# Performance work log

Hardware: AMD Instinct MI355X
Metric: run time of the kernel (lower is better)

## Reference

```python
import jax, jax.numpy as jnp
import numpy as np

N = 100000
E = 1600000
G = 2048          # number of graphs in the batch
HEADS = 4
HID = 16          # per-head channels
IN_CH = 128
D = HEADS * HID   # 64, concat output width per layer
NEG_SLOPE = 0.2


def _gat_layer(x, src, dst, W, a_src, a_dst, bias):
    # x: [N, Fin], W: [Fin, H*C], a_src/a_dst: [H, C], bias: [H*C]
    h = (x @ W).reshape(N, HEADS, HID)                      # [N, H, C]
    al_s = jnp.einsum('nhc,hc->nh', h, a_src)               # [N, H]
    al_d = jnp.einsum('nhc,hc->nh', h, a_dst)               # [N, H]
    e = jax.nn.leaky_relu(al_s[src] + al_d[dst], NEG_SLOPE) # [E+N, H]
    # segment softmax over incoming edges of each destination node
    m = jax.ops.segment_max(e, dst, num_segments=N)         # [N, H]
    e = jnp.exp(e - m[dst])
    s = jax.ops.segment_sum(e, dst, num_segments=N)
    alpha = e / (s[dst] + 1e-16)                            # [E+N, H]
    msg = h[src] * alpha[..., None]                         # [E+N, H, C]
    out = jax.ops.segment_sum(msg, dst, num_segments=N)     # [N, H, C]
    return out.reshape(N, D) + bias


def setup_inputs() -> dict:
    key = jax.random.key(0)
    ks = jax.random.split(key, 16)
    x = jax.random.normal(ks[0], (N, IN_CH), dtype=jnp.float32)
    edge_index = jax.random.randint(ks[1], (2, E), 0, N, dtype=jnp.int64)
    batch = jnp.sort(jax.random.randint(ks[2], (N,), 0, G, dtype=jnp.int64))
    inp = {'x': x, 'edge_index': edge_index, 'batch': batch}
    fins = [IN_CH, D, D]
    for i, fin in enumerate(fins):
        kk = jax.random.split(ks[3 + i], 4)
        sc = 1.0 / np.sqrt(fin)
        inp[f'W{i}'] = jax.random.normal(kk[0], (fin, D), dtype=jnp.float32) * sc
        inp[f'as{i}'] = jax.random.normal(kk[1], (HEADS, HID), dtype=jnp.float32) * 0.1
        inp[f'ad{i}'] = jax.random.normal(kk[2], (HEADS, HID), dtype=jnp.float32) * 0.1
        inp[f'b{i}'] = jnp.zeros((D,), dtype=jnp.float32)
    inp['head_w'] = jax.random.normal(ks[10], (1, D), dtype=jnp.float32) * (1.0 / np.sqrt(D))
    inp['head_b'] = jnp.zeros((1,), dtype=jnp.float32)
    return inp


def reference(x, edge_index, batch,
              W0, as0, ad0, b0,
              W1, as1, ad1, b1,
              W2, as2, ad2, b2,
              head_w, head_b):
    # PyG GATConv adds self-loops by default
    loops = jnp.arange(N, dtype=edge_index.dtype)
    src = jnp.concatenate([edge_index[0], loops])
    dst = jnp.concatenate([edge_index[1], loops])
    layers = [(W0, as0, ad0, b0), (W1, as1, ad1, b1), (W2, as2, ad2, b2)]
    h = x.astype(jnp.float32)
    for (W, a_s, a_d, b) in layers:
        h = _gat_layer(h, src, dst, W, a_s, a_d, b)
        h = jax.nn.relu(h)  # dropout p=0.0 -> identity
    pooled = jax.ops.segment_sum(h, batch, num_segments=G)  # [G, D]
    out = pooled @ head_w.T + head_b                         # [G, 1]
    return out.reshape(-1)                                   # out_dim == 1 -> flatten
```

## Files before the change

### kernel.cpp

```cpp
#include <hip/hip_runtime.h>
#include <hip/hip_bf16.h>
#include <cstdint>
#include <cstddef>

#define NN 100000
#define EE 1600000
#define GG 2048
#define EN (EE + NN)

constexpr int NB_SCAN = (NN + 255) / 256;

__device__ __forceinline__ float lrelu(float v) { return v > 0.f ? v : 0.2f * v; }

__global__ void k_count(const int* __restrict__ ei, int* __restrict__ deg,
                        int* __restrict__ rank) {
    int i = blockIdx.x * blockDim.x + threadIdx.x;
    if (i >= EN) return;
    int d = (i < EE) ? ei[EE + i] : (i - EE);
    rank[i] = atomicAdd(&deg[d], 1);
}

__global__ void k_scan1(const int* __restrict__ deg, int* __restrict__ offs,
                        int* __restrict__ bsums) {
    __shared__ int tmp[256];
    int tid = threadIdx.x;
    int i = blockIdx.x * 256 + tid;
    int v = (i < NN) ? deg[i] : 0;
    tmp[tid] = v; __syncthreads();
    for (int off = 1; off < 256; off <<= 1) {
        int t = (tid >= off) ? tmp[tid - off] : 0;
        __syncthreads();
        tmp[tid] += t;
        __syncthreads();
    }
    if (i < NN) offs[i] = tmp[tid] - v;
    if (tid == 255) bsums[blockIdx.x] = tmp[255];
}

__global__ void k_scan2(int* __restrict__ bsums) {
    __shared__ int tmp[512];
    int tid = threadIdx.x;
    int v = (tid < NB_SCAN) ? bsums[tid] : 0;
    tmp[tid] = v; __syncthreads();
    for (int off = 1; off < 512; off <<= 1) {
        int t = (tid >= off) ? tmp[tid - off] : 0;
        __syncthreads();
        tmp[tid] += t;
        __syncthreads();
    }
    if (tid < NB_SCAN) bsums[tid] = tmp[tid] - v;
}

__global__ void k_scan3(int* __restrict__ offs, const int* __restrict__ bsums) {
    int i = blockIdx.x * 256 + threadIdx.x;
    if (i < NN) offs[i] += bsums[blockIdx.x];
}

__global__ void k_scatter(const int* __restrict__ ei, const int* __restrict__ offs,
                          const int* __restrict__ rank, int* __restrict__ col) {
    int i = blockIdx.x * blockDim.x + threadIdx.x;
    if (i >= EN) return;
    int s, d;
    if (i < EE) { s = ei[i]; d = ei[EE + i]; } else { s = d = i - EE; }
    col[offs[d] + rank[i]] = s;
}

template <int FIN>
__global__ __launch_bounds__(256) void k_gemm(const float* __restrict__ X,
                                              const float* __restrict__ W,
                                              const float* __restrict__ asrc,
                                              const float* __restrict__ adst,
                                              float* __restrict__ H,
                                              float* __restrict__ als,
                                              float* __restrict__ ald) {
    int j  = threadIdx.x & 63;
    int ty = threadIdx.x >> 6;
    int row = __builtin_amdgcn_readfirstlane(blockIdx.x * 16 + ty * 4);
    const float* x0 = X + (size_t)row * FIN;
    const float* x1 = x0 + FIN;
    const float* x2 = x1 + FIN;
    const float* x3 = x2 + FIN;
    float a0 = 0.f, a1 = 0.f, a2 = 0.f, a3 = 0.f;
#pragma unroll
    for (int k = 0; k < FIN; k += 4) {
        float4 xa = *(const float4*)(x0 + k);
        float4 xb = *(const float4*)(x1 + k);
        float4 xc = *(const float4*)(x2 + k);
        float4 xd = *(const float4*)(x3 + k);
        float w0 = W[(k + 0) * 64 + j];
        float w1 = W[(k + 1) * 64 + j];
        float w2 = W[(k + 2) * 64 + j];
        float w3 = W[(k + 3) * 64 + j];
        a0 += xa.x * w0 + xa.y * w1 + xa.z * w2 + xa.w * w3;
        a1 += xb.x * w0 + xb.y * w1 + xb.z * w2 + xb.w * w3;
        a2 += xc.x * w0 + xc.y * w1 + xc.z * w2 + xc.w * w3;
        a3 += xd.x * w0 + xd.y * w1 + xd.z * w2 + xd.w * w3;
    }
    H[(size_t)(row + 0) * 64 + j] = a0;
    H[(size_t)(row + 1) * 64 + j] = a1;
    H[(size_t)(row + 2) * 64 + j] = a2;
    H[(size_t)(row + 3) * 64 + j] = a3;
    float asj = asrc[j], adj = adst[j];
    float accs[4] = {a0, a1, a2, a3};
#pragma unroll
    for (int r = 0; r < 4; r++) {
        float vs = accs[r] * asj;
        float vd = accs[r] * adj;
#pragma unroll
        for (int off = 8; off > 0; off >>= 1) {
            vs += __shfl_xor(vs, off, 64);
            vd += __shfl_xor(vd, off, 64);
        }
        if ((j & 15) == 0) {
            int h = j >> 4;
            als[(size_t)(row + r) * 4 + h] = vs;
            ald[(size_t)(row + r) * 4 + h] = vd;
        }
    }
}

#define LWPITCH 260
__global__ __launch_bounds__(256) void k_agg(
    const float* __restrict__ H, const float* __restrict__ als,
    const float* __restrict__ ald, const int* __restrict__ offs,
    const int* __restrict__ deg, const int* __restrict__ col,
    const float* __restrict__ bias, float* __restrict__ Hout,
    const int* __restrict__ batch, const float* __restrict__ hw,
    float* __restrict__ out, int last) {
    __shared__ float lws[16 * LWPITCH];
    int tid = threadIdx.x;
    int g = tid >> 4;
    int l = tid & 15;
    int n = blockIdx.x * 16 + g;
    int start = offs[n];
    int len = deg[n];
    float4 ad4 = ((const float4*)ald)[n];
    int hsel = l >> 2;
    const float4* Hp = (const float4*)H + l;
    const int* cp = col + start;
    float* lw = lws + g * LWPITCH;
    bool fast = (len <= 64);
    float inv = 1.f;

    if (fast) {
        float ev[4][4];
        bool  vld[4];
        float m0 = -1e30f, m1 = -1e30f, m2 = -1e30f, m3 = -1e30f;
#pragma unroll
        for (int it = 0; it < 4; it++) {
            int e = l + it * 16;
            vld[it] = (e < len);
            int s = vld[it] ? cp[e] : 0;
            float4 a = ((const float4*)als)[s];
            ev[it][0] = lrelu(a.x + ad4.x); ev[it][1] = lrelu(a.y + ad4.y);
            ev[it][2] = lrelu(a.z + ad4.z); ev[it][3] = lrelu(a.w + ad4.w);
            if (vld[it]) {
                m0 = fmaxf(m0, ev[it][0]); m1 = fmaxf(m1, ev[it][1]);
                m2 = fmaxf(m2, ev[it][2]); m3 = fmaxf(m3, ev[it][3]);
            }
        }
#pragma unroll
        for (int off = 8; off > 0; off >>= 1) {
            m0 = fmaxf(m0, __shfl_xor(m0, off, 16));
            m1 = fmaxf(m1, __shfl_xor(m1, off, 16));
            m2 = fmaxf(m2, __shfl_xor(m2, off, 16));
            m3 = fmaxf(m3, __shfl_xor(m3, off, 16));
        }
        float s0 = 0.f, s1 = 0.f, s2 = 0.f, s3 = 0.f;
#pragma unroll
        for (int it = 0; it < 4; it++) {
            int e = l + it * 16;
            float w0 = vld[it] ? __expf(ev[it][0] - m0) : 0.f;
            float w1 = vld[it] ? __expf(ev[it][1] - m1) : 0.f;
            float w2 = vld[it] ? __expf(ev[it][2] - m2) : 0.f;
            float w3 = vld[it] ? __expf(ev[it][3] - m3) : 0.f;
            s0 += w0; s1 += w1; s2 += w2; s3 += w3;
            ((float4*)(lw + e * 4))[0] = make_float4(w0, w1, w2, w3);
        }
#pragma unroll
        for (int off = 8; off > 0; off >>= 1) {
            s0 += __shfl_xor(s0, off, 16); s1 += __shfl_xor(s1, off, 16);
            s2 += __shfl_xor(s2, off, 16); s3 += __shfl_xor(s3, off, 16);
        }
        float smh = hsel == 0 ? s0 : hsel == 1 ? s1 : hsel == 2 ? s2 : s3;
        inv = 1.f / (smh + 1e-16f);
    }

    __syncthreads();

    float4 acc = {0.f, 0.f, 0.f, 0.f};
    if (fast) {
        int e = 0;
        for (; e + 8 <= len; e += 8) {
            int i0 = cp[e + 0], i1 = cp[e + 1], i2 = cp[e + 2], i3 = cp[e + 3];
            int i4 = cp[e + 4], i5 = cp[e + 5], i6 = cp[e + 6], i7 = cp[e + 7];
            float w0 = lw[(e + 0) * 4 + hsel], w1 = lw[(e + 1) * 4 + hsel];
            float w2 = lw[(e + 2) * 4 + hsel], w3 = lw[(e + 3) * 4 + hsel];
            float w4 = lw[(e + 4) * 4 + hsel], w5 = lw[(e + 5) * 4 + hsel];
            float w6 = lw[(e + 6) * 4 + hsel], w7 = lw[(e + 7) * 4 + hsel];
            float4 h0 = Hp[(size_t)i0 * 16];
            float4 h1 = Hp[(size_t)i1 * 16];
            float4 h2 = Hp[(size_t)i2 * 16];
            float4 h3 = Hp[(size_t)i3 * 16];
            float4 h4 = Hp[(size_t)i4 * 16];
            float4 h5 = Hp[(size_t)i5 * 16];
            float4 h6 = Hp[(size_t)i6 * 16];
            float4 h7 = Hp[(size_t)i7 * 16];
            acc.x += w0 * h0.x + w1 * h1.x + w2 * h2.x + w3 * h3.x
                   + w4 * h4.x + w5 * h5.x + w6 * h6.x + w7 * h7.x;
            acc.y += w0 * h0.y + w1 * h1.y + w2 * h2.y + w3 * h3.y
                   + w4 * h4.y + w5 * h5.y + w6 * h6.y + w7 * h7.y;
            acc.z += w0 * h0.z + w1 * h1.z + w2 * h2.z + w3 * h3.z
                   + w4 * h4.z + w5 * h5.z + w6 * h6.z + w7 * h7.z;
            acc.w += w0 * h0.w + w1 * h1.w + w2 * h2.w + w3 * h3.w
                   + w4 * h4.w + w5 * h5.w + w6 * h6.w + w7 * h7.w;
        }
        for (; e + 4 <= len; e += 4) {
            int i0 = cp[e + 0], i1 = cp[e + 1], i2 = cp[e + 2], i3 = cp[e + 3];
            float w0 = lw[(e + 0) * 4 + hsel], w1 = lw[(e + 1) * 4 + hsel];
            float w2 = lw[(e + 2) * 4 + hsel], w3 = lw[(e + 3) * 4 + hsel];
            float4 h0 = Hp[(size_t)i0 * 16];
            float4 h1 = Hp[(size_t)i1 * 16];
            float4 h2 = Hp[(size_t)i2 * 16];
            float4 h3 = Hp[(size_t)i3 * 16];
            acc.x += w0 * h0.x + w1 * h1.x + w2 * h2.x + w3 * h3.x;
            acc.y += w0 * h0.y + w1 * h1.y + w2 * h2.y + w3 * h3.y;
            acc.z += w0 * h0.z + w1 * h1.z + w2 * h2.z + w3 * h3.z;
            acc.w += w0 * h0.w + w1 * h1.w + w2 * h2.w + w3 * h3.w;
        }
        for (; e < len; e++) {
            int i0 = cp[e];
            float w0 = lw[e * 4 + hsel];
            float4 h0 = Hp[(size_t)i0 * 16];
            acc.x += w0 * h0.x; acc.y += w0 * h0.y;
            acc.z += w0 * h0.z; acc.w += w0 * h0.w;
        }
    } else {
        float m0 = -1e30f, m1 = -1e30f, m2 = -1e30f, m3 = -1e30f;
        for (int e = l; e < len; e += 16) {
            int s = cp[e];
            float4 a = ((const float4*)als)[s];
            m0 = fmaxf(m0, lrelu(a.x + ad4.x)); m1 = fmaxf(m1, lrelu(a.y + ad4.y));
            m2 = fmaxf(m2, lrelu(a.z + ad4.z)); m3 = fmaxf(m3, lrelu(a.w + ad4.w));
        }
#pragma unroll
        for (int off = 8; off > 0; off >>= 1) {
            m0 = fmaxf(m0, __shfl_xor(m0, off, 16));
            m1 = fmaxf(m1, __shfl_xor(m1, off, 16));
            m2 = fmaxf(m2, __shfl_xor(m2, off, 16));
            m3 = fmaxf(m3, __shfl_xor(m3, off, 16));
        }
        float s0 = 0.f, s1 = 0.f, s2 = 0.f, s3 = 0.f;
        for (int e = l; e < len; e += 16) {
            int s = cp[e];
            float4 a = ((const float4*)als)[s];
            s0 += __expf(lrelu(a.x + ad4.x) - m0); s1 += __expf(lrelu(a.y + ad4.y) - m1);
            s2 += __expf(lrelu(a.z + ad4.z) - m2); s3 += __expf(lrelu(a.w + ad4.w) - m3);
        }
#pragma unroll
        for (int off = 8; off > 0; off >>= 1) {
            s0 += __shfl_xor(s0, off, 16); s1 += __shfl_xor(s1, off, 16);
            s2 += __shfl_xor(s2, off, 16); s3 += __shfl_xor(s3, off, 16);
        }
        float mh = hsel == 0 ? m0 : hsel == 1 ? m1 : hsel == 2 ? m2 : m3;
        float sh = hsel == 0 ? s0 : hsel == 1 ? s1 : hsel == 2 ? s2 : s3;
        float ih = 1.f / (sh + 1e-16f);
        float ah = hsel == 0 ? ad4.x : hsel == 1 ? ad4.y : hsel == 2 ? ad4.z : ad4.w;
        for (int e = 0; e < len; e++) {
            int s = cp[e];
            float alpha = __expf(lrelu(als[(size_t)s * 4 + hsel] + ah) - mh) * ih;
            float4 h0 = Hp[(size_t)s * 16];
            acc.x += alpha * h0.x; acc.y += alpha * h0.y;
            acc.z += alpha * h0.z; acc.w += alpha * h0.w;
        }
        inv = 1.f;
    }

    float4 b4 = ((const float4*)bias)[l];
    float4 o4;
    o4.x = fmaxf(acc.x * inv + b4.x, 0.f);
    o4.y = fmaxf(acc.y * inv + b4.y, 0.f);
    o4.z = fmaxf(acc.z * inv + b4.z, 0.f);
    o4.w = fmaxf(acc.w * inv + b4.w, 0.f);
    if (!last) {
        ((float4*)Hout)[(size_t)n * 16 + l] = o4;
    } else {
        float4 w4 = ((const float4*)hw)[l];
        float t = o4.x * w4.x + o4.y * w4.y + o4.z * w4.z + o4.w * w4.w;
#pragma unroll
        for (int off = 8; off > 0; off >>= 1) t += __shfl_xor(t, off, 16);
        if (l == 0) atomicAdd(&out[batch[n]], t);
    }
}

__global__ void k_out_init(const float* __restrict__ head_b, float* __restrict__ out) {
    int g = blockIdx.x * blockDim.x + threadIdx.x;
    if (g < GG) out[g] = head_b[0];
}

extern "C" void kernel_launch(void* const* d_in, const int* in_sizes, int n_in,
                              void* d_out, int out_size, void* d_ws, size_t ws_size,
                              hipStream_t stream) {
    const float* x     = (const float*)d_in[0];
    const int*   ei    = (const int*)d_in[1];
    const int*   batch = (const int*)d_in[2];
    const float* Wm[3] = {(const float*)d_in[3], (const float*)d_in[7],  (const float*)d_in[11]};
    const float* As[3] = {(const float*)d_in[4], (const float*)d_in[8],  (const float*)d_in[12]};
    const float* Ad[3] = {(const float*)d_in[5], (const float*)d_in[9],  (const float*)d_in[13]};
    const float* Bb[3] = {(const float*)d_in[6], (const float*)d_in[10], (const float*)d_in[14]};
    const float* hw = (const float*)d_in[15];
    const float* hb = (const float*)d_in[16];
    float* out = (float*)d_out;

    uint8_t* w = (uint8_t*)d_ws;
    auto alloc = [&](size_t bytes) -> void* {
        void* p = (void*)w;
        w += (bytes + 255) & ~(size_t)255;
        return p;
    };
    float* H     = (float*)alloc((size_t)NN * 64 * 4);
    float* Bf    = (float*)alloc((size_t)NN * 64 * 4);
    float* als   = (float*)alloc((size_t)NN * 4 * 4);
    float* ald   = (float*)alloc((size_t)NN * 4 * 4);
    int*   deg   = (int*)alloc((size_t)NN * 4);
    int*   offs  = (int*)alloc((size_t)NN * 4);
    int*   rank  = (int*)alloc((size_t)EN * 4);
    int*   col   = (int*)alloc((size_t)EN * 4);
    int*   bsums = (int*)alloc((size_t)((NB_SCAN + 63) & ~63) * 4);

    hipMemsetAsync(deg, 0, (size_t)NN * 4, stream);

    int eb = (EN + 255) / 256;
    k_count  <<<eb, 256, 0, stream>>>(ei, deg, rank);
    k_scan1  <<<NB_SCAN, 256, 0, stream>>>(deg, offs, bsums);
    k_scan2  <<<1, 512, 0, stream>>>(bsums);
    k_scan3  <<<NB_SCAN, 256, 0, stream>>>(offs, bsums);
    k_scatter<<<eb, 256, 0, stream>>>(ei, offs, rank, col);
    k_out_init<<<(GG + 255) / 256, 256, 0, stream>>>(hb, out);

    const float* cur_in = x;
    for (int L = 0; L < 3; L++) {
        if (L == 0)
            k_gemm<128><<<NN / 16, 256, 0, stream>>>(
                cur_in, Wm[L], As[L], Ad[L], H, als, ald);
        else
            k_gemm<64><<<NN / 16, 256, 0, stream>>>(
                cur_in, Wm[L], As[L], Ad[L], H, als, ald);
        k_agg <<<NN / 16, 256, 0, stream>>>(
            H, als, ald, offs, deg, col, Bb[L], Bf, batch, hw, out, (L == 2) ? 1 : 0);
        cur_in = Bf;
    }
}
```

Baseline: 542.9 us.

## Split attention aggregation into separate alpha and gather kernels

Splits the fused aggregation kernel in two. k_alpha computes the normalized softmax weights for every edge and writes them to a global per-edge alpha buffer. k_gather then reads those weights to do the weighted neighbor sum, without shared memory or __syncthreads. This removes the shared-memory staging and barrier and should give the gather kernel better occupancy. In exchange it adds a kernel launch per layer and an extra global write and read of a 27 MB alpha array. The rank buffer is aliased onto the alpha buffer to save workspace.

```diff
diff --git a/kernel.cpp b/kernel.cpp
--- a/kernel.cpp
+++ b/kernel.cpp
@@ -119,30 +119,20 @@
     }
 }
 
-#define LWPITCH 260
-__global__ __launch_bounds__(256) void k_agg(
-    const float* __restrict__ H, const float* __restrict__ als,
-    const float* __restrict__ ald, const int* __restrict__ offs,
-    const int* __restrict__ deg, const int* __restrict__ col,
-    const float* __restrict__ bias, float* __restrict__ Hout,
-    const int* __restrict__ batch, const float* __restrict__ hw,
-    float* __restrict__ out, int last) {
-    __shared__ float lws[16 * LWPITCH];
+__global__ __launch_bounds__(256) void k_alpha(
+    const float* __restrict__ als, const float* __restrict__ ald,
+    const int* __restrict__ offs, const int* __restrict__ deg,
+    const int* __restrict__ col, float* __restrict__ alpha) {
     int tid = threadIdx.x;
-    int g = tid >> 4;
-    int l = tid & 15;
+    int g = tid >> 4, l = tid & 15;
     int n = blockIdx.x * 16 + g;
     int start = offs[n];
     int len = deg[n];
     float4 ad4 = ((const float4*)ald)[n];
-    int hsel = l >> 2;
-    const float4* Hp = (const float4*)H + l;
     const int* cp = col + start;
-    float* lw = lws + g * LWPITCH;
-    bool fast = (len <= 64);
-    float inv = 1.f;
-
-    if (fast) {
+    float4* ap = (float4*)alpha + start;
+
+    if (len <= 64) {
         float ev[4][4];
         bool  vld[4];
         float m0 = -1e30f, m1 = -1e30f, m2 = -1e30f, m3 = -1e30f;
@@ -166,74 +156,29 @@
             m2 = fmaxf(m2, __shfl_xor(m2, off, 16));
             m3 = fmaxf(m3, __shfl_xor(m3, off, 16));
         }
+        float w[4][4];
         float s0 = 0.f, s1 = 0.f, s2 = 0.f, s3 = 0.f;
+#pragma unroll
+        for (int it = 0; it < 4; it++) {
+            w[it][0] = vld[it] ? __expf(ev[it][0] - m0) : 0.f;
+            w[it][1] = vld[it] ? __expf(ev[it][1] - m1) : 0.f;
+            w[it][2] = vld[it] ? __expf(ev[it][2] - m2) : 0.f;
+            w[it][3] = vld[it] ? __expf(ev[it][3] - m3) : 0.f;
+            s0 += w[it][0]; s1 += w[it][1]; s2 += w[it][2]; s3 += w[it][3];
+        }
+#pragma unroll
+        for (int off = 8; off > 0; off >>= 1) {
+            s0 += __shfl_xor(s0, off, 16); s1 += __shfl_xor(s1, off, 16);
+            s2 += __shfl_xor(s2, off, 16); s3 += __shfl_xor(s3, off, 16);
+        }
+        float i0 = 1.f / (s0 + 1e-16f), i1 = 1.f / (s1 + 1e-16f);
+        float i2 = 1.f / (s2 + 1e-16f), i3 = 1.f / (s3 + 1e-16f);
 #pragma unroll
         for (int it = 0; it < 4; it++) {
             int e = l + it * 16;
-            float w0 = vld[it] ? __expf(ev[it][0] - m0) : 0.f;
-            float w1 = vld[it] ? __expf(ev[it][1] - m1) : 0.f;
-            float w2 = vld[it] ? __expf(ev[it][2] - m2) : 0.f;
-            float w3 = vld[it] ? __expf(ev[it][3] - m3) : 0.f;
-            s0 += w0; s1 += w1; s2 += w2; s3 += w3;
-            ((float4*)(lw + e * 4))[0] = make_float4(w0, w1, w2, w3);
-        }
-#pragma unroll
-        for (int off = 8; off > 0; off >>= 1) {
-            s0 += __shfl_xor(s0, off, 16); s1 += __shfl_xor(s1, off, 16);
-            s2 += __shfl_xor(s2, off, 16); s3 += __shfl_xor(s3, off, 16);
-        }
-        float smh = hsel == 0 ? s0 : hsel == 1 ? s1 : hsel == 2 ? s2 : s3;
-        inv = 1.f / (smh + 1e-16f);
-    }
-
-    __syncthreads();
-
-    float4 acc = {0.f, 0.f, 0.f, 0.f};
-    if (fast) {
-        int e = 0;
-        for (; e + 8 <= len; e += 8) {
-            int i0 = cp[e + 0], i1 = cp[e + 1], i2 = cp[e + 2], i3 = cp[e + 3];
-            int i4 = cp[e + 4], i5 = cp[e + 5], i6 = cp[e + 6], i7 = cp[e + 7];
-            float w0 = lw[(e + 0) * 4 + hsel], w1 = lw[(e + 1) * 4 + hsel];
-            float w2 = lw[(e + 2) * 4 + hsel], w3 = lw[(e + 3) * 4 + hsel];
-            float w4 = lw[(e + 4) * 4 + hsel], w5 = lw[(e + 5) * 4 + hsel];
-            float w6 = lw[(e + 6) * 4 + hsel], w7 = lw[(e + 7) * 4 + hsel];
-            float4 h0 = Hp[(size_t)i0 * 16];
-            float4 h1 = Hp[(size_t)i1 * 16];
-            float4 h2 = Hp[(size_t)i2 * 16];
-            float4 h3 = Hp[(size_t)i3 * 16];
-            float4 h4 = Hp[(size_t)i4 * 16];
-            float4 h5 = Hp[(size_t)i5 * 16];
-            float4 h6 = Hp[(size_t)i6 * 16];
-            float4 h7 = Hp[(size_t)i7 * 16];
-            acc.x += w0 * h0.x + w1 * h1.x + w2 * h2.x + w3 * h3.x
-                   + w4 * h4.x + w5 * h5.x + w6 * h6.x + w7 * h7.x;
-            acc.y += w0 * h0.y + w1 * h1.y + w2 * h2.y + w3 * h3.y
-                   + w4 * h4.y + w5 * h5.y + w6 * h6.y + w7 * h7.y;
-            acc.z += w0 * h0.z + w1 * h1.z + w2 * h2.z + w3 * h3.z
-                   + w4 * h4.z + w5 * h5.z + w6 * h6.z + w7 * h7.z;
-            acc.w += w0 * h0.w + w1 * h1.w + w2 * h2.w + w3 * h3.w
-                   + w4 * h4.w + w5 * h5.w + w6 * h6.w + w7 * h7.w;
-        }
-        for (; e + 4 <= len; e += 4) {
-            int i0 = cp[e + 0], i1 = cp[e + 1], i2 = cp[e + 2], i3 = cp[e + 3];
-            float w0 = lw[(e + 0) * 4 + hsel], w1 = lw[(e + 1) * 4 + hsel];
-            float w2 = lw[(e + 2) * 4 + hsel], w3 = lw[(e + 3) * 4 + hsel];
-            float4 h0 = Hp[(size_t)i0 * 16];
-            float4 h1 = Hp[(size_t)i1 * 16];
-            float4 h2 = Hp[(size_t)i2 * 16];
-            float4 h3 = Hp[(size_t)i3 * 16];
-            acc.x += w0 * h0.x + w1 * h1.x + w2 * h2.x + w3 * h3.x;
-            acc.y += w0 * h0.y + w1 * h1.y + w2 * h2.y + w3 * h3.y;
-            acc.z += w0 * h0.z + w1 * h1.z + w2 * h2.z + w3 * h3.z;
-            acc.w += w0 * h0.w + w1 * h1.w + w2 * h2.w + w3 * h3.w;
-        }
-        for (; e < len; e++) {
-            int i0 = cp[e];
-            float w0 = lw[e * 4 + hsel];
-            float4 h0 = Hp[(size_t)i0 * 16];
-            acc.x += w0 * h0.x; acc.y += w0 * h0.y;
-            acc.z += w0 * h0.z; acc.w += w0 * h0.w;
+            if (vld[it])
+                ap[e] = make_float4(w[it][0] * i0, w[it][1] * i1,
+                                    w[it][2] * i2, w[it][3] * i3);
         }
     } else {
         float m0 = -1e30f, m1 = -1e30f, m2 = -1e30f, m3 = -1e30f;
@@ -262,26 +207,86 @@
             s0 += __shfl_xor(s0, off, 16); s1 += __shfl_xor(s1, off, 16);
             s2 += __shfl_xor(s2, off, 16); s3 += __shfl_xor(s3, off, 16);
         }
-        float mh = hsel == 0 ? m0 : hsel == 1 ? m1 : hsel == 2 ? m2 : m3;
-        float sh = hsel == 0 ? s0 : hsel == 1 ? s1 : hsel == 2 ? s2 : s3;
-        float ih = 1.f / (sh + 1e-16f);
-        float ah = hsel == 0 ? ad4.x : hsel == 1 ? ad4.y : hsel == 2 ? ad4.z : ad4.w;
-        for (int e = 0; e < len; e++) {
+        float i0 = 1.f / (s0 + 1e-16f), i1 = 1.f / (s1 + 1e-16f);
+        float i2 = 1.f / (s2 + 1e-16f), i3 = 1.f / (s3 + 1e-16f);
+        for (int e = l; e < len; e += 16) {
             int s = cp[e];
-            float alpha = __expf(lrelu(als[(size_t)s * 4 + hsel] + ah) - mh) * ih;
-            float4 h0 = Hp[(size_t)s * 16];
-            acc.x += alpha * h0.x; acc.y += alpha * h0.y;
-            acc.z += alpha * h0.z; acc.w += alpha * h0.w;
-        }
-        inv = 1.f;
-    }
-
+            float4 a = ((const float4*)als)[s];
+            ap[e] = make_float4(__expf(lrelu(a.x + ad4.x) - m0) * i0,
+                                __expf(lrelu(a.y + ad4.y) - m1) * i1,
+                                __expf(lrelu(a.z + ad4.z) - m2) * i2,
+                                __expf(lrelu(a.w + ad4.w) - m3) * i3);
+        }
+    }
+}
+
+__global__ __launch_bounds__(256) void k_gather(
+    const float* __restrict__ H, const float* __restrict__ alpha,
+    const int* __restrict__ offs, const int* __restrict__ deg,
+    const int* __restrict__ col, const float* __restrict__ bias,
+    float* __restrict__ Hout, const int* __restrict__ batch,
+    const float* __restrict__ hw, float* __restrict__ out, int last) {
+    int tid = threadIdx.x;
+    int g = tid >> 4, l = tid & 15;
+    int n = blockIdx.x * 16 + g;
+    int start = offs[n];
+    int len = deg[n];
+    int hsel = l >> 2;
+    const float4* Hp = (const float4*)H + l;
+    const int*    cp = col + start;
+    const float*  ap = alpha + (size_t)start * 4 + hsel;
+    float4 acc = {0.f, 0.f, 0.f, 0.f};
+    int e = 0;
+    for (; e + 8 <= len; e += 8) {
+        int i0 = cp[e + 0], i1 = cp[e + 1], i2 = cp[e + 2], i3 = cp[e + 3];
+        int i4 = cp[e + 4], i5 = cp[e + 5], i6 = cp[e + 6], i7 = cp[e + 7];
+        float w0 = ap[(e + 0) * 4], w1 = ap[(e + 1) * 4];
+        float w2 = ap[(e + 2) * 4], w3 = ap[(e + 3) * 4];
+        float w4 = ap[(e + 4) * 4], w5 = ap[(e + 5) * 4];
+        float w6 = ap[(e + 6) * 4], w7 = ap[(e + 7) * 4];
+        float4 h0 = Hp[(size_t)i0 * 16];
+        float4 h1 = Hp[(size_t)i1 * 16];
+        float4 h2 = Hp[(size_t)i2 * 16];
+        float4 h3 = Hp[(size_t)i3 * 16];
+        float4 h4 = Hp[(size_t)i4 * 16];
+        float4 h5 = Hp[(size_t)i5 * 16];
+        float4 h6 = Hp[(size_t)i6 * 16];
+        float4 h7 = Hp[(size_t)i7 * 16];
+        acc.x += w0 * h0.x + w1 * h1.x + w2 * h2.x + w3 * h3.x
+               + w4 * h4.x + w5 * h5.x + w6 * h6.x + w7 * h7.x;
+        acc.y += w0 * h0.y + w1 * h1.y + w2 * h2.y + w3 * h3.y
+               + w4 * h4.y + w5 * h5.y + w6 * h6.y + w7 * h7.y;
+        acc.z += w0 * h0.z + w1 * h1.z + w2 * h2.z + w3 * h3.z
+               + w4 * h4.z + w5 * h5.z + w6 * h6.z + w7 * h7.z;
+        acc.w += w0 * h0.w + w1 * h1.w + w2 * h2.w + w3 * h3.w
+               + w4 * h4.w + w5 * h5.w + w6 * h6.w + w7 * h7.w;
+    }
+    for (; e + 4 <= len; e += 4) {
+        int i0 = cp[e + 0], i1 = cp[e + 1], i2 = cp[e + 2], i3 = cp[e + 3];
+        float w0 = ap[(e + 0) * 4], w1 = ap[(e + 1) * 4];
+        float w2 = ap[(e + 2) * 4], w3 = ap[(e + 3) * 4];
+        float4 h0 = Hp[(size_t)i0 * 16];
+        float4 h1 = Hp[(size_t)i1 * 16];
+        float4 h2 = Hp[(size_t)i2 * 16];
+        float4 h3 = Hp[(size_t)i3 * 16];
+        acc.x += w0 * h0.x + w1 * h1.x + w2 * h2.x + w3 * h3.x;
+        acc.y += w0 * h0.y + w1 * h1.y + w2 * h2.y + w3 * h3.y;
+        acc.z += w0 * h0.z + w1 * h1.z + w2 * h2.z + w3 * h3.z;
+        acc.w += w0 * h0.w + w1 * h1.w + w2 * h2.w + w3 * h3.w;
+    }
+    for (; e < len; e++) {
+        int i0 = cp[e];
+        float w0 = ap[e * 4];
+        float4 h0 = Hp[(size_t)i0 * 16];
+        acc.x += w0 * h0.x; acc.y += w0 * h0.y;
+        acc.z += w0 * h0.z; acc.w += w0 * h0.w;
+    }
     float4 b4 = ((const float4*)bias)[l];
     float4 o4;
-    o4.x = fmaxf(acc.x * inv + b4.x, 0.f);
-    o4.y = fmaxf(acc.y * inv + b4.y, 0.f);
-    o4.z = fmaxf(acc.z * inv + b4.z, 0.f);
-    o4.w = fmaxf(acc.w * inv + b4.w, 0.f);
+    o4.x = fmaxf(acc.x + b4.x, 0.f);
+    o4.y = fmaxf(acc.y + b4.y, 0.f);
+    o4.z = fmaxf(acc.z + b4.z, 0.f);
+    o4.w = fmaxf(acc.w + b4.w, 0.f);
     if (!last) {
         ((float4*)Hout)[(size_t)n * 16 + l] = o4;
     } else {
@@ -324,9 +329,10 @@
     float* ald   = (float*)alloc((size_t)NN * 4 * 4);
     int*   deg   = (int*)alloc((size_t)NN * 4);
     int*   offs  = (int*)alloc((size_t)NN * 4);
-    int*   rank  = (int*)alloc((size_t)EN * 4);
     int*   col   = (int*)alloc((size_t)EN * 4);
+    float* alpha = (float*)alloc((size_t)EN * 4 * 4);
     int*   bsums = (int*)alloc((size_t)((NB_SCAN + 63) & ~63) * 4);
+    int*   rank  = (int*)alpha;
 
     hipMemsetAsync(deg, 0, (size_t)NN * 4, stream);
 
@@ -346,8 +352,9 @@
         else
             k_gemm<64><<<NN / 16, 256, 0, stream>>>(
                 cur_in, Wm[L], As[L], Ad[L], H, als, ald);
-        k_agg <<<NN / 16, 256, 0, stream>>>(
-            H, als, ald, offs, deg, col, Bb[L], Bf, batch, hw, out, (L == 2) ? 1 : 0);
+        k_alpha <<<NN / 16, 256, 0, stream>>>(als, ald, offs, deg, col, alpha);
+        k_gather<<<NN / 16, 256, 0, stream>>>(
+            H, alpha, offs, deg, col, Bb[L], Bf, batch, hw, out, (L == 2) ? 1 : 0);
         cur_in = Bf;
     }
 }
```

Result: slower. 593.3 us (+9.3%).
